# Performance work log

Hardware: AMD Instinct MI355X
Metric: run time of the kernel (lower is better)

The kernel has to match this reference:

```python
import jax, jax.numpy as jnp
import numpy as np

B, S, W = 16, 512, 5
H, E, V = 512, 256, 100000


def setup_inputs() -> dict:
    key = jax.random.key(0)
    ks = jax.random.split(key, 20)
    inp = {
        "hiddens": jax.random.normal(ks[0], (B, S, H), jnp.float32),
        "masks": jax.random.randint(ks[1], (B, S), 0, 2, jnp.int32),
        "begins": jax.random.randint(ks[2], (B, S, W), 0, V, jnp.int32),
        "begin_lens": jax.random.randint(ks[3], (B, S), 0, W + 1, jnp.int32),
        "middles": jax.random.randint(ks[4], (B, S, W), 0, V, jnp.int32),
        "middle_lens": jax.random.randint(ks[5], (B, S), 0, W + 1, jnp.int32),
        "ends": jax.random.randint(ks[6], (B, S, W), 0, V, jnp.int32),
        "end_lens": jax.random.randint(ks[7], (B, S), 0, W + 1, jnp.int32),
        # parameters
        "emb": jax.random.normal(ks[8], (V, E), jnp.float32) * 0.02,
        "W_hidden": jax.random.normal(ks[9], (H, 3 * H), jnp.float32) * (1.0 / np.sqrt(H)),
        "b_hidden": jnp.zeros((3 * H,), jnp.float32),
        "W_begin": jax.random.normal(ks[10], (E, 2 * H), jnp.float32) * (1.0 / np.sqrt(E)),
        "b_begin": jnp.zeros((2 * H,), jnp.float32),
        "W_middle": jax.random.normal(ks[11], (E, 2 * H), jnp.float32) * (1.0 / np.sqrt(E)),
        "b_middle": jnp.zeros((2 * H,), jnp.float32),
        "W_end": jax.random.normal(ks[12], (E, 2 * H), jnp.float32) * (1.0 / np.sqrt(E)),
        "b_end": jnp.zeros((2 * H,), jnp.float32),
        "W_gate": jax.random.normal(ks[13], (H, 9), jnp.float32) * (1.0 / np.sqrt(H)),
        "b_gate": jnp.zeros((9,), jnp.float32),
    }
    return inp


def _len_mask(lens, w):
    # True where the lattice candidate is valid (mimics _make_mask's 1s)
    return jnp.arange(w)[None, None, :] < lens[:, :, None]


def _gates(hiddens, masks, W_gate, b_gate):
    b, s, _ = hiddens.shape
    lmr = hiddens @ W_gate + b_gate                      # (B,S,9)
    left, mid, right = jnp.split(lmr, 3, axis=-1)        # each (B,S,3)
    g = jax.nn.sigmoid(left[:, :-2] + mid[:, 1:-1] + right[:, 2:])  # (B,S-2,3)
    ones = jnp.ones((b, 1), g.dtype)
    zeros = jnp.zeros((b, 1), g.dtype)
    begin_g = jnp.concatenate([ones, g[..., 0], ones], axis=1)
    mid_g = jnp.concatenate([zeros, g[..., 1], zeros], axis=1)
    end_g = jnp.concatenate([ones, g[..., 2], ones], axis=1)
    pad = masks == 0
    z = jnp.zeros((), g.dtype)
    return (jnp.where(pad, z, begin_g), jnp.where(pad, z, mid_g), jnp.where(pad, z, end_g))


def reference(hiddens, masks, begins, begin_lens, middles, middle_lens, ends, end_lens,
              emb, W_hidden, b_hidden, W_begin, b_begin, W_middle, b_middle,
              W_end, b_end, W_gate, b_gate):
    w = begins.shape[-1]
    begin_m = _len_mask(begin_lens, w)
    middle_m = _len_mask(middle_lens, w)
    end_m = _len_mask(end_lens, w)

    begin_kv = emb[begins] @ W_begin + b_begin           # (B,S,W,2H)
    middle_kv = emb[middles] @ W_middle + b_middle
    end_kv = emb[ends] @ W_end + b_end

    query, hidden_key, hidden_value = jnp.split(hiddens @ W_hidden + b_hidden, 3, axis=-1)
    bg, mg, eg = _gates(hiddens, masks, W_gate, b_gate)
    begin_kv = bg[:, :, None, None] * begin_kv
    middle_kv = mg[:, :, None, None] * middle_kv
    end_kv = eg[:, :, None, None] * end_kv

    kv = jnp.concatenate([begin_kv, middle_kv, end_kv], axis=-2)   # (B,S,3W,2H)
    h = hiddens.shape[-1]
    keys, values = jnp.split(kv, 2, axis=-1)
    keys = jnp.concatenate([hidden_key[:, :, None, :], keys], axis=-2)     # (B,S,1+3W,H)
    values = jnp.concatenate([hidden_value[:, :, None, :], values], axis=-2)

    # combined mask: True entries get -1e10 (faithful to masked_fill_(masks, -1e10))
    score_mask = jnp.concatenate(
        [(masks != 0)[:, :, None], begin_m, middle_m, end_m], axis=-1)     # (B,S,1+3W)

    scores = jnp.einsum("bsh,bskh->bsk", query, keys)
    scores = jnp.where(score_mask, jnp.asarray(-1e10, scores.dtype), scores)
    weights = jax.nn.softmax(scores, axis=-1)
    return jnp.einsum("bsk,bskh->bsh", weights, values)
```

## Files before the change

kernel.cpp:

```cpp
#include <hip/hip_runtime.h>
#include <cstdint>
#include <cstddef>


typedef unsigned short u16;
typedef _Float16 f16;
typedef __attribute__((ext_vector_type(8))) f16 f16x8;
typedef __attribute__((ext_vector_type(4))) float f32x4;

#define MROWS 8192
#define SS 512

static __device__ __forceinline__ u16 f2h(float x) {
  f16 h = (f16)x;
  return __builtin_bit_cast(u16, h);
}
static __device__ __forceinline__ float h2f(u16 h) {
  return (float)__builtin_bit_cast(f16, h);
}
static __device__ __forceinline__ float sigm(float x) { return 1.f / (1.f + __expf(-x)); }

static __device__ __forceinline__ void gl2lds(const u16* g, u16* l) {
  __builtin_amdgcn_global_load_lds(
      (const __attribute__((address_space(1))) unsigned int*)g,
      (__attribute__((address_space(3))) unsigned int*)l, 16, 0, 0);
}

__global__ __launch_bounds__(256) void prep_all(
    const float* __restrict__ X, const float* __restrict__ Wg,
    const float* __restrict__ bg, const float* __restrict__ Wh,
    const float* __restrict__ Wb, const float* __restrict__ Wm,
    const float* __restrict__ We, const float* __restrict__ bb,
    const float* __restrict__ bm, const float* __restrict__ be,
    const float* __restrict__ bh, const int* __restrict__ masks,
    u16* __restrict__ Xh, float* __restrict__ lmr, float* __restrict__ s0,
    u16* __restrict__ Breg, u16* __restrict__ Acat, u16* __restrict__ Whq,
    u16* __restrict__ WvT, float* __restrict__ bcat, float* __restrict__ u,
    float* __restrict__ cbuf, int* __restrict__ idx, int* __restrict__ perm,
    int* __restrict__ cnts) {
  __shared__ float shmem[4608];
#define TI(r, c) shmem[(r)*65 + (c)]
  const int b = blockIdx.x;
  const int t = threadIdx.x;
  if (b < 64) {
    int k0 = (b & 7) * 64;
    int n0 = (b >> 3) * 64;
#pragma unroll
    for (int i = 0; i < 16; i++) {
      int li = i * 256 + t; int r = li >> 6, c = li & 63;
      TI(r, c) = Wh[(size_t)(k0 + r) * 1536 + 1024 + n0 + c];
    }
    __syncthreads();
#pragma unroll
    for (int i = 0; i < 16; i++) {
      int li = i * 256 + t; int r = li >> 6, c = li & 63;
      Breg[(size_t)(512 + n0 + r) * 512 + k0 + c] = f2h(TI(c, r));
    }
  } else if (b < 128) {
#pragma unroll
    for (int i = 0; i < 4; i++) {
      int q4 = (b - 64) * 1024 + t * 4 + i;
      int k = q4 >> 7;
      int c4 = (q4 & 127) * 4;
      float4 vq = *(const float4*)(Wh + (size_t)k * 1536 + c4);
      float4 vk = *(const float4*)(Wh + (size_t)k * 1536 + 512 + c4);
      ushort4 qh, kh;
      qh.x = f2h(vq.x); qh.y = f2h(vq.y); qh.z = f2h(vq.z); qh.w = f2h(vq.w);
      kh.x = f2h(vk.x); kh.y = f2h(vk.y); kh.z = f2h(vk.z); kh.w = f2h(vk.w);
      size_t o = (size_t)k * 512 + c4;
      *(ushort4*)(Whq + o) = qh;
      *(ushort4*)(Acat + o) = kh;
    }
  } else if (b < 576) {
    int tid = (b - 128) * 256 + t;
    int n = tid >> 7;
    int kq = (tid & 127) * 4;
    float4 v;
    if (n < 768) {
      int ty = n >> 8, c = n & 255;
      const float* src = (ty == 0 ? Wb : ty == 1 ? Wm : We) + (size_t)c * 1024 + kq;
      v = *(const float4*)src;
    } else if (n < 771) {
      int ty = n - 768;
      const float* src = (ty == 0 ? bb : ty == 1 ? bm : be) + kq;
      v = *(const float4*)src;
    } else {
      v = make_float4(0.f, 0.f, 0.f, 0.f);
    }
    ushort4 h; h.x = f2h(v.x); h.y = f2h(v.y); h.z = f2h(v.z); h.w = f2h(v.w);
    ((ushort4*)(Acat + (size_t)512 * 512))[tid] = h;
  } else if (b < 672) {
    int idx2 = b - 576;
    int ty = idx2 >> 5;
    int rem = idx2 & 31;
    int c0 = (rem & 3) * 64;
    int n0 = (rem >> 2) * 64;
    const float* Wsrc = ty == 0 ? Wb : ty == 1 ? Wm : We;
#pragma unroll
    for (int i = 0; i < 16; i++) {
      int li = i * 256 + t; int r = li >> 6, c = li & 63;
      TI(r, c) = Wsrc[(size_t)(c0 + r) * 1024 + 512 + n0 + c];
    }
    __syncthreads();
#pragma unroll
    for (int i = 0; i < 16; i++) {
      int li = i * 256 + t; int r = li >> 6, c = li & 63;
      WvT[(size_t)(n0 + r) * 768 + ty * 256 + c0 + c] = f2h(TI(c, r));
    }
  } else if (b < 1028) {
    const int lane = t & 63;
    const int widx = (b - 672) * 4 + (t >> 6);
    const int c = lane * 8;
    if (widx < 896) {
      int n = widx;
      float acc = 0.f;
      if (n < 771) {
        const float* src;
        if (n < 768) {
          int ty = n >> 8, ce = n & 255;
          src = (ty == 0 ? Wb : ty == 1 ? Wm : We) + (size_t)ce * 1024 + c;
        } else {
          int ty = n - 768;
          src = (ty == 0 ? bb : ty == 1 ? bm : be) + c;
        }
        float4 a0 = *(const float4*)src;
        float4 a1 = *(const float4*)(src + 4);
        float4 b0 = *(const float4*)(bh + c);
        float4 b1 = *(const float4*)(bh + c + 4);
        acc = a0.x * b0.x + a0.y * b0.y + a0.z * b0.z + a0.w * b0.w +
              a1.x * b1.x + a1.y * b1.y + a1.z * b1.z + a1.w * b1.w;
      }
#pragma unroll
      for (int o = 32; o > 0; o >>= 1) acc += __shfl_xor(acc, o);
      if (lane == 0) bcat[512 + n] = acc;
    } else if (widx < 1408) {
      int k = widx - 896;
      const float* wr = Wh + (size_t)k * 1536;
      float4 a0 = *(const float4*)(wr + c);
      float4 a1 = *(const float4*)(wr + c + 4);
      float4 a2 = *(const float4*)(wr + 512 + c);
      float4 a3 = *(const float4*)(wr + 512 + c + 4);
      float4 b0 = *(const float4*)(bh + 512 + c);
      float4 b1 = *(const float4*)(bh + 512 + c + 4);
      float4 b2 = *(const float4*)(bh + c);
      float4 b3 = *(const float4*)(bh + c + 4);
      float acc = a0.x * b0.x + a0.y * b0.y + a0.z * b0.z + a0.w * b0.w +
                  a1.x * b1.x + a1.y * b1.y + a1.z * b1.z + a1.w * b1.w +
                  a2.x * b2.x + a2.y * b2.y + a2.z * b2.z + a2.w * b2.w +
                  a3.x * b3.x + a3.y * b3.y + a3.z * b3.z + a3.w * b3.w;
#pragma unroll
      for (int o = 32; o > 0; o >>= 1) acc += __shfl_xor(acc, o);
      if (lane == 0) u[k] = acc;
    } else if (widx == 1408) {
      float4 b0 = *(const float4*)(bh + c);
      float4 b1 = *(const float4*)(bh + c + 4);
      float4 b2 = *(const float4*)(bh + 512 + c);
      float4 b3 = *(const float4*)(bh + 512 + c + 4);
      float acc = b0.x * b2.x + b0.y * b2.y + b0.z * b2.z + b0.w * b2.w +
                  b1.x * b3.x + b1.y * b3.y + b1.z * b3.z + b1.w * b3.w;
#pragma unroll
      for (int o = 32; o > 0; o >>= 1) acc += __shfl_xor(acc, o);
      if (lane == 0) cbuf[0] = acc;
    } else if (widx < 1417) {
      int i = (widx - 1409) * 64 + lane;
      bcat[i] = bh[1024 + i];
    }
  } else if (b < 1540) {
    const int xb = b - 1028;
    if (xb < 32) s0[xb * 256 + t] = 0.f;
    for (int i = t; i < 4608; i += 256) shmem[i] = Wg[i];
    __syncthreads();
    const int lane = t & 63, wid = t >> 6;
#pragma unroll
    for (int it = 0; it < 4; it++) {
      int pos = xb * 16 + it * 4 + wid;
      const float* x = X + (size_t)pos * 512 + lane * 8;
      float4 x0 = *(const float4*)x;
      float4 x1 = *(const float4*)(x + 4);
      float xs[8] = {x0.x, x0.y, x0.z, x0.w, x1.x, x1.y, x1.z, x1.w};
      ushort4 h0, h1;
      h0.x = f2h(xs[0]); h0.y = f2h(xs[1]); h0.z = f2h(xs[2]); h0.w = f2h(xs[3]);
      h1.x = f2h(xs[4]); h1.y = f2h(xs[5]); h1.z = f2h(xs[6]); h1.w = f2h(xs[7]);
      ((ushort4*)Xh)[pos * 128 + lane * 2] = h0;
      ((ushort4*)Xh)[pos * 128 + lane * 2 + 1] = h1;
      float p[9];
#pragma unroll
      for (int c = 0; c < 9; c++) p[c] = 0.f;
      const float* wrow = shmem + (lane * 8) * 9;
#pragma unroll
      for (int j = 0; j < 8; j++)
#pragma unroll
        for (int c = 0; c < 9; c++) p[c] += xs[j] * wrow[j * 9 + c];
#pragma unroll
      for (int c = 0; c < 9; c++)
#pragma unroll
        for (int o = 32; o > 0; o >>= 1) p[c] += __shfl_xor(p[c], o);
      if (lane == 0) {
#pragma unroll
        for (int c = 0; c < 9; c++) lmr[(size_t)pos * 9 + c] = p[c] + bg[c];
      }
    }
  } else {
    const int lane = t & 63;
    const int pos = (b - 1540) * 256 + t;
    bool is0 = masks[pos] == 0;
    unsigned long long bal = __ballot(is0);
    unsigned long long below = (lane == 0) ? 0ull : (~0ull >> (64 - lane));
    int rank0 = __popcll(bal & below);
    int rank1 = __popcll((~bal) & below);
    int n0w = __popcll(bal);
    int base0 = 0, base1 = 0;
    if (lane == 0) {
      base0 = atomicAdd(&cnts[0], n0w);
      base1 = atomicAdd(&cnts[1], 64 - n0w);
    }
    base0 = __shfl(base0, 0);
    base1 = __shfl(base1, 0);
    int slot = is0 ? (base0 + rank0) : (8191 - (base1 + rank1));
    perm[pos] = slot;
    idx[slot] = pos;
  }
#undef TI
}

template <int MODE>
__global__ __launch_bounds__(256) void gemm_k(
    const u16* __restrict__ A, const u16* __restrict__ Bt,
    const float* __restrict__ ubias, const float* __restrict__ bcat,
    float* __restrict__ Cf, u16* __restrict__ Cb, int Kdim,
    const u16* __restrict__ Xh, float* __restrict__ s0c,
    const int* __restrict__ idx, const int* __restrict__ cnts,
    const float4* __restrict__ sc4, const u16* __restrict__ HPb,
    const float* __restrict__ bb, const float* __restrict__ bm,
    const float* __restrict__ be) {
  __shared__ __align__(16) u16 As[2 * 128 * 32];
  __shared__ __align__(16) u16 Bs[2 * 128 * 32];

  const int t = threadIdx.x;
  const int lane = t & 63;
  const int wid = t >> 6;
  const int m0 = blockIdx.x * 128;
  const int n0 = blockIdx.y * 128;

  bool remap = false;
  if constexpr (MODE == 0) {
    const int cnt0 = cnts[0];
    if (blockIdx.y < 4) {
      if (m0 >= cnt0) return;
      remap = true;
    } else if (blockIdx.y >= 8) {
      if (m0 + 128 <= cnt0) return;
      remap = true;
    }
  }

  int ra0 = m0 + (t >> 2), ra1 = m0 + 64 + (t >> 2);
  if (MODE == 0 && remap) { ra0 = idx[ra0]; ra1 = idx[ra1]; }
  const int rb0 = n0 + (t >> 2), rb1 = n0 + 64 + (t >> 2);
  const int koff = (t & 3) * 8;
  const int lds0 = (t >> 2) * 32 + koff;
  const int lds1 = 2048 + lds0;

  const int wm = (wid & 1) * 64;
  const int wn = (wid >> 1) * 64;
  const int fr = lane & 15;
  const int kq = (lane >> 4) * 8;

  f32x4 acc[4][4];
#pragma unroll
  for (int i = 0; i < 4; i++)
#pragma unroll
    for (int j = 0; j < 4; j++) acc[i][j] = (f32x4){0.f, 0.f, 0.f, 0.f};

  for (int k0 = 0; k0 < Kdim; k0 += 64) {
    __syncthreads();
#pragma unroll
    for (int pn = 0; pn < 2; pn++) {
      const int kb = k0 + pn * 32 + koff;
      gl2lds(&A[(size_t)ra0 * Kdim + kb], &As[pn * 4096 + lds0]);
      gl2lds(&A[(size_t)ra1 * Kdim + kb], &As[pn * 4096 + lds1]);
      gl2lds(&Bt[(size_t)rb0 * Kdim + kb], &Bs[pn * 4096 + lds0]);
      gl2lds(&Bt[(size_t)rb1 * Kdim + kb], &Bs[pn * 4096 + lds1]);
    }
    __syncthreads();
#pragma unroll
    for (int pn = 0; pn < 2; pn++) {
      f16x8 av[4], bv[4];
#pragma unroll
      for (int i = 0; i < 4; i++) {
        av[i] = *(const f16x8*)&As[pn * 4096 + (wm + i * 16 + fr) * 32 + kq];
        bv[i] = *(const f16x8*)&Bs[pn * 4096 + (wn + i * 16 + fr) * 32 + kq];
      }
#pragma unroll
      for (int mt = 0; mt < 4; mt++)
#pragma unroll
        for (int nt = 0; nt < 4; nt++)
          acc[mt][nt] = __builtin_amdgcn_mfma_f32_16x16x32_f16(
              av[mt], bv[nt], acc[mt][nt], 0, 0, 0);
    }
  }

  const int r0 = (lane >> 4) * 4;
  if constexpr (MODE == 0) {
    if (blockIdx.y < 4) {
      float pl[4][4];
      int xrow[4][4];
#pragma unroll
      for (int mt = 0; mt < 4; mt++)
#pragma unroll
        for (int r = 0; r < 4; r++) {
          pl[mt][r] = 0.f;
          xrow[mt][r] = idx[m0 + wm + mt * 16 + r0 + r];
        }
#pragma unroll
      for (int mt = 0; mt < 4; mt++)
#pragma unroll
        for (int nt = 0; nt < 4; nt++) {
          int col = n0 + wn + nt * 16 + fr;
          float bv2 = ubias[col];
#pragma unroll
          for (int r = 0; r < 4; r++)
            pl[mt][r] += (acc[mt][nt][r] + bv2) *
                         h2f(Xh[(size_t)xrow[mt][r] * 512 + col]);
        }
#pragma unroll
      for (int mt = 0; mt < 4; mt++)
#pragma unroll
        for (int r = 0; r < 4; r++) {
          float p = pl[mt][r];
          p += __shfl_xor(p, 1);
          p += __shfl_xor(p, 2);
          p += __shfl_xor(p, 4);
          p += __shfl_xor(p, 8);
          if (fr == r) {
            int slot = m0 + wm + mt * 16 + r0 + r;
            atomicAdd(&s0c[slot], p);
          }
        }
      return;
    }
    if (blockIdx.y < 8) {
#pragma unroll
      for (int mt = 0; mt < 4; mt++)
#pragma unroll
        for (int nt = 0; nt < 4; nt++) {
          int col = n0 - 512 + wn + nt * 16 + fr;
          float bv2 = bcat[col];
#pragma unroll
          for (int r = 0; r < 4; r++) {
            int row = m0 + wm + mt * 16 + r0 + r;
            Cb[(size_t)row * 1408 + col] = f2h(acc[mt][nt][r] + bv2);
          }
        }
    } else {
#pragma unroll
      for (int mt = 0; mt < 4; mt++)
#pragma unroll
        for (int nt = 0; nt < 4; nt++) {
          int pcol = n0 - 1024 + wn + nt * 16 + fr;
          float bv2 = bcat[512 + pcol];
#pragma unroll
          for (int r = 0; r < 4; r++) {
            int slot = m0 + wm + mt * 16 + r0 + r;
            Cb[(size_t)slot * 1408 + 512 + pcol] = f2h(acc[mt][nt][r] + bv2);
          }
        }
    }
  } else if constexpr (MODE == 1) {
#pragma unroll
    for (int mt = 0; mt < 4; mt++)
#pragma unroll
      for (int nt = 0; nt < 4; nt++) {
        int col = n0 + wn + nt * 16 + fr;
#pragma unroll
        for (int r = 0; r < 4; r++) {
          int row = m0 + wm + mt * 16 + r0 + r;
          int orow = row < 512 ? row : row + 512;
          Cb[(size_t)orow * 512 + col] = f2h(acc[mt][nt][r]);
        }
      }
  } else {
#pragma unroll
    for (int mt = 0; mt < 4; mt++)
#pragma unroll
      for (int nt = 0; nt < 4; nt++) {
        int col = n0 + wn + nt * 16 + fr;
        float b0 = bb[512 + col];
        float b1 = bm[512 + col];
        float b2 = be[512 + col];
#pragma unroll
        for (int r = 0; r < 4; r++) {
          int row = m0 + wm + mt * 16 + r0 + r;
          float4 s = sc4[row];
          float hv = h2f(HPb[(size_t)row * 1408 + col]);
          Cf[(size_t)row * 512 + col] =
              s.x * hv + s.y * b0 + s.z * b1 + s.w * b2 + acc[mt][nt][r];
        }
      }
  }
}

__global__ __launch_bounds__(256) void attn_kernel(
    const int* __restrict__ masks, const int* __restrict__ begins,
    const int* __restrict__ blens, const int* __restrict__ middles,
    const int* __restrict__ mlens, const int* __restrict__ ends,
    const int* __restrict__ elens, const float* __restrict__ emb,
    const u16* __restrict__ HPb, const float* __restrict__ lmr,
    const float* __restrict__ s0buf, const float* __restrict__ cbuf,
    const int* __restrict__ perm, float4* __restrict__ sc4,
    u16* __restrict__ Ebar) {
  const int t = threadIdx.x;
  const int lane = t & 63;
  const int wid = t >> 6;
  const int pos = blockIdx.x * 4 + wid;
  const int mask = masks[pos];
  const int slot = perm[pos];
  u16* erow = Ebar + (size_t)pos * 768;

  int l0 = min(blens[pos], 5), l1 = min(mlens[pos], 5), l2 = min(elens[pos], 5);
  int nv = l0 + l1 + l2;

  if (mask == 0) {
    float s0 = s0buf[slot] + cbuf[0];
    int ninv = 15 - nv;
    float w0;
    if (ninv == 0) {
      w0 = 1.f;
    } else {
      float Mx = fmaxf(s0, 0.f);
      float e0 = __expf(s0 - Mx);
      w0 = e0 / (e0 + (float)ninv * __expf(-Mx));
    }
    if (lane == 0) sc4[pos] = make_float4(w0, 0.f, 0.f, 0.f);
    ushort4 zz; zz.x = zz.y = zz.z = zz.w = 0;
    *(ushort4*)(erow + 0 * 256 + lane * 4) = zz;
    *(ushort4*)(erow + 1 * 256 + lane * 4) = zz;
    *(ushort4*)(erow + 2 * 256 + lane * 4) = zz;
  } else {
    const int s = pos & (SS - 1);
    float g[3];
    if (s == 0 || s == SS - 1) {
      g[0] = 1.f; g[1] = 0.f; g[2] = 1.f;
    } else {
      const float* p0 = lmr + (size_t)(pos - 1) * 9;
      const float* p1 = lmr + (size_t)pos * 9;
      const float* p2 = lmr + (size_t)(pos + 1) * 9;
      g[0] = sigm(p0[0] + p1[3] + p2[6]);
      g[1] = sigm(p0[1] + p1[4] + p2[7]);
      g[2] = sigm(p0[2] + p1[5] + p2[8]);
    }
    const bool deg = (nv == 15);
    int l[3] = {l0, l1, l2};
    if (deg) { l[0] = 0; l[1] = 0; l[2] = 0; }

    float4 Pt[3];
    float qb[3];
    if (!deg) {
      const u16* prow = HPb + (size_t)slot * 1408 + 512;
#pragma unroll
      for (int ty = 0; ty < 3; ty++) {
        ushort4 pu = *(const ushort4*)(prow + ty * 256 + lane * 4);
        Pt[ty].x = h2f(pu.x); Pt[ty].y = h2f(pu.y);
        Pt[ty].z = h2f(pu.z); Pt[ty].w = h2f(pu.w);
        qb[ty] = h2f(prow[768 + ty]);
      }
    }
    const int* idxp[3];
    idxp[0] = begins + (size_t)pos * 5;
    idxp[1] = middles + (size_t)pos * 5;
    idxp[2] = ends + (size_t)pos * 5;

    float4 ev[3][5];
    float scv[3][5];
    float Mx = deg ? 0.f : -3.0e38f;
#pragma unroll
    for (int ty = 0; ty < 3; ty++) {
#pragma unroll
      for (int w = 0; w < 5; w++) {
        bool act = (w >= l[ty]);
        if (act) {
          ev[ty][w] = *(const float4*)(emb + (size_t)idxp[ty][w] * 256 + lane * 4);
          float sv = 0.f;
          if (!deg) {
            float4 e = ev[ty][w];
            float d = Pt[ty].x * e.x + Pt[ty].y * e.y + Pt[ty].z * e.z + Pt[ty].w * e.w;
#pragma unroll
            for (int o = 32; o > 0; o >>= 1) d += __shfl_xor(d, o);
            sv = g[ty] * (d + qb[ty]);
          }
          scv[ty][w] = sv;
          Mx = fmaxf(Mx, sv);
        }
      }
    }
    float wts0 = deg ? 1.f : 0.f;
    float zs = wts0;
    float wts[3][5];
#pragma unroll
    for (int ty = 0; ty < 3; ty++)
#pragma unroll
      for (int w = 0; w < 5; w++) {
        bool act = (w >= l[ty]);
        float wv = act ? __expf(scv[ty][w] - Mx) : 0.f;
        wts[ty][w] = wv;
        zs += wv;
      }
    float inv = 1.f / zs;
    float alpha[3];
#pragma unroll
    for (int ty = 0; ty < 3; ty++) {
      float ax = 0.f, ay = 0.f, az = 0.f, aw = 0.f, asum = 0.f;
#pragma unroll
      for (int w = 0; w < 5; w++) {
        if (w >= l[ty]) {
          float wk = wts[ty][w];
          asum += wk;
          ax += wk * ev[ty][w].x;
          ay += wk * ev[ty][w].y;
          az += wk * ev[ty][w].z;
          aw += wk * ev[ty][w].w;
        }
      }
      float sg = g[ty] * inv;
      alpha[ty] = sg * asum;
      ushort4 h;
      h.x = f2h(ax * sg); h.y = f2h(ay * sg); h.z = f2h(az * sg); h.w = f2h(aw * sg);
      *(ushort4*)(erow + ty * 256 + lane * 4) = h;
    }
    if (lane == 0) sc4[pos] = make_float4(wts0 * inv, alpha[0], alpha[1], alpha[2]);
  }
}

extern "C" void kernel_launch(void* const* d_in, const int* in_sizes, int n_in,
                              void* d_out, int out_size, void* d_ws, size_t ws_size,
                              hipStream_t stream) {
  const float* hiddens = (const float*)d_in[0];
  const int* masks = (const int*)d_in[1];
  const int* begins = (const int*)d_in[2];
  const int* blens = (const int*)d_in[3];
  const int* middles = (const int*)d_in[4];
  const int* mlens = (const int*)d_in[5];
  const int* ends = (const int*)d_in[6];
  const int* elens = (const int*)d_in[7];
  const float* emb = (const float*)d_in[8];
  const float* Wh = (const float*)d_in[9];
  const float* bh = (const float*)d_in[10];
  const float* Wb = (const float*)d_in[11];
  const float* bb = (const float*)d_in[12];
  const float* Wm = (const float*)d_in[13];
  const float* bm = (const float*)d_in[14];
  const float* We = (const float*)d_in[15];
  const float* be = (const float*)d_in[16];
  const float* Wg = (const float*)d_in[17];
  const float* bg = (const float*)d_in[18];
  float* out = (float*)d_out;

  char* ws = (char*)d_ws;
  size_t off = 0;
  auto alloc = [&](size_t bytes) -> char* {
    char* p = ws + off;
    off += (bytes + 255) & ~(size_t)255;
    return p;
  };
  u16* Xh = (u16*)alloc((size_t)8192 * 512 * 2);
  u16* Whq = (u16*)alloc((size_t)512 * 512 * 2);
  u16* Acat = (u16*)alloc((size_t)1408 * 512 * 2);
  u16* Breg = (u16*)alloc((size_t)1920 * 512 * 2);
  u16* WvT = (u16*)alloc((size_t)512 * 768 * 2);
  u16* HPb = (u16*)alloc((size_t)8192 * 1408 * 2);
  float* lmr = (float*)alloc((size_t)8192 * 9 * 4);
  float* s0c = (float*)alloc((size_t)8192 * 4);
  float* bcat = (float*)alloc((size_t)1408 * 4);
  float* u = (float*)alloc((size_t)512 * 4);
  float* cbuf = (float*)alloc((size_t)4);
  float* sc4 = (float*)alloc((size_t)8192 * 4 * 4);
  u16* Ebar = (u16*)alloc((size_t)8192 * 768 * 2);
  int* idx = (int*)alloc((size_t)8192 * 4);
  int* perm = (int*)alloc((size_t)8192 * 4);
  int* cnts = (int*)alloc((size_t)256);
  if (off > ws_size) return;

  hipMemsetAsync(cnts, 0, 8, stream);
  prep_all<<<1572, 256, 0, stream>>>(hiddens, Wg, bg, Wh, Wb, Wm, We, bb, bm, be,
                                     bh, masks, Xh, lmr, s0c, Breg, Acat, Whq,
                                     WvT, bcat, u, cbuf, idx, perm, cnts);
  gemm_k<1><<<dim3(11, 4), 256, 0, stream>>>(
      Acat, Whq, nullptr, nullptr, nullptr, Breg, 512, nullptr, nullptr,
      nullptr, nullptr, nullptr, nullptr, nullptr, nullptr, nullptr);
  gemm_k<0><<<dim3(64, 15), 256, 0, stream>>>(
      Xh, Breg, u, bcat, nullptr, HPb, 512, Xh, s0c, idx, cnts,
      nullptr, nullptr, nullptr, nullptr, nullptr);
  attn_kernel<<<2048, 256, 0, stream>>>(masks, begins, blens, middles, mlens,
                                        ends, elens, emb, HPb, lmr, s0c, cbuf,
                                        perm, (float4*)sc4, Ebar);
  gemm_k<2><<<dim3(64, 4), 256, 0, stream>>>(
      Ebar, WvT, nullptr, nullptr, out, nullptr, 768, nullptr, nullptr,
      nullptr, nullptr, (const float4*)sc4, HPb, bb, bm, be);
}
```

Baseline: 278.9 us.

## Double-buffer GEMM k-loop and halve N tile for final GEMM

Replaces the load-all-then-compute k-loop (two 32-wide k-chunks per iteration with two barriers) with a ping-pong double buffer, so the next 32-wide k slice is fetched into LDS while MFMAs run on the current one. This applies to all three GEMM modes. The final projection GEMM (MODE 2) also switches to 64-column N tiles with a 64x8 grid, doubling block count for better CU occupancy. In exchange it does more global A-tile loads per output, and each iteration now carries less compute to hide latency.

```diff
diff --git a/kernel.cpp b/kernel.cpp
--- a/kernel.cpp
+++ b/kernel.cpp
@@ -233,14 +233,16 @@
     const float4* __restrict__ sc4, const u16* __restrict__ HPb,
     const float* __restrict__ bb, const float* __restrict__ bm,
     const float* __restrict__ be) {
+  constexpr int BROWS = (MODE == 2) ? 64 : 128;
+  constexpr int NT = (MODE == 2) ? 2 : 4;
   __shared__ __align__(16) u16 As[2 * 128 * 32];
-  __shared__ __align__(16) u16 Bs[2 * 128 * 32];
+  __shared__ __align__(16) u16 Bs[2 * BROWS * 32];
 
   const int t = threadIdx.x;
   const int lane = t & 63;
   const int wid = t >> 6;
   const int m0 = blockIdx.x * 128;
-  const int n0 = blockIdx.y * 128;
+  const int n0 = blockIdx.y * BROWS;
 
   bool remap = false;
   if constexpr (MODE == 0) {
@@ -262,43 +264,50 @@
   const int lds1 = 2048 + lds0;
 
   const int wm = (wid & 1) * 64;
-  const int wn = (wid >> 1) * 64;
+  const int wn = (wid >> 1) * (NT * 16);
   const int fr = lane & 15;
   const int kq = (lane >> 4) * 8;
 
-  f32x4 acc[4][4];
+  f32x4 acc[4][NT];
 #pragma unroll
   for (int i = 0; i < 4; i++)
 #pragma unroll
-    for (int j = 0; j < 4; j++) acc[i][j] = (f32x4){0.f, 0.f, 0.f, 0.f};
-
-  for (int k0 = 0; k0 < Kdim; k0 += 64) {
+    for (int j = 0; j < NT; j++) acc[i][j] = (f32x4){0.f, 0.f, 0.f, 0.f};
+
+  auto STAGE = [&](int kb, int buf) {
+    gl2lds(&A[(size_t)ra0 * Kdim + kb], &As[buf * 4096 + lds0]);
+    gl2lds(&A[(size_t)ra1 * Kdim + kb], &As[buf * 4096 + lds1]);
+    gl2lds(&Bt[(size_t)rb0 * Kdim + kb], &Bs[buf * (BROWS * 32) + lds0]);
+    if constexpr (BROWS == 128)
+      gl2lds(&Bt[(size_t)rb1 * Kdim + kb], &Bs[buf * (BROWS * 32) + lds1]);
+  };
+  auto COMPUTE = [&](int buf) {
+    f16x8 av[4], bv[NT];
+#pragma unroll
+    for (int i = 0; i < 4; i++)
+      av[i] = *(const f16x8*)&As[buf * 4096 + (wm + i * 16 + fr) * 32 + kq];
+#pragma unroll
+    for (int j = 0; j < NT; j++)
+      bv[j] = *(const f16x8*)&Bs[buf * (BROWS * 32) + (wn + j * 16 + fr) * 32 + kq];
+#pragma unroll
+    for (int mt = 0; mt < 4; mt++)
+#pragma unroll
+      for (int nt = 0; nt < NT; nt++)
+        acc[mt][nt] = __builtin_amdgcn_mfma_f32_16x16x32_f16(
+            av[mt], bv[nt], acc[mt][nt], 0, 0, 0);
+  };
+
+  STAGE(koff, 0);
+  __syncthreads();
+  const int nk = Kdim >> 5;
+  int buf = 0;
+  for (int ki = 0; ki < nk - 1; ++ki) {
+    STAGE((ki + 1) * 32 + koff, buf ^ 1);
+    COMPUTE(buf);
     __syncthreads();
-#pragma unroll
-    for (int pn = 0; pn < 2; pn++) {
-      const int kb = k0 + pn * 32 + koff;
-      gl2lds(&A[(size_t)ra0 * Kdim + kb], &As[pn * 4096 + lds0]);
-      gl2lds(&A[(size_t)ra1 * Kdim + kb], &As[pn * 4096 + lds1]);
-      gl2lds(&Bt[(size_t)rb0 * Kdim + kb], &Bs[pn * 4096 + lds0]);
-      gl2lds(&Bt[(size_t)rb1 * Kdim + kb], &Bs[pn * 4096 + lds1]);
-    }
-    __syncthreads();
-#pragma unroll
-    for (int pn = 0; pn < 2; pn++) {
-      f16x8 av[4], bv[4];
-#pragma unroll
-      for (int i = 0; i < 4; i++) {
-        av[i] = *(const f16x8*)&As[pn * 4096 + (wm + i * 16 + fr) * 32 + kq];
-        bv[i] = *(const f16x8*)&Bs[pn * 4096 + (wn + i * 16 + fr) * 32 + kq];
-      }
-#pragma unroll
-      for (int mt = 0; mt < 4; mt++)
-#pragma unroll
-        for (int nt = 0; nt < 4; nt++)
-          acc[mt][nt] = __builtin_amdgcn_mfma_f32_16x16x32_f16(
-              av[mt], bv[nt], acc[mt][nt], 0, 0, 0);
-    }
+    buf ^= 1;
   }
+  COMPUTE(buf);
 
   const int r0 = (lane >> 4) * 4;
   if constexpr (MODE == 0) {
@@ -383,7 +392,7 @@
 #pragma unroll
     for (int mt = 0; mt < 4; mt++)
 #pragma unroll
-      for (int nt = 0; nt < 4; nt++) {
+      for (int nt = 0; nt < NT; nt++) {
         int col = n0 + wn + nt * 16 + fr;
         float b0 = bb[512 + col];
         float b1 = bm[512 + col];
@@ -593,7 +602,7 @@
   attn_kernel<<<2048, 256, 0, stream>>>(masks, begins, blens, middles, mlens,
                                         ends, elens, emb, HPb, lmr, s0c, cbuf,
                                         perm, (float4*)sc4, Ebar);
-  gemm_k<2><<<dim3(64, 4), 256, 0, stream>>>(
+  gemm_k<2><<<dim3(64, 8), 256, 0, stream>>>(
       Ebar, WvT, nullptr, nullptr, out, nullptr, 768, nullptr, nullptr,
       nullptr, nullptr, (const float4*)sc4, HPb, bb, bm, be);
 }
```

Result: slower. 287.7 us (+3.1%).
